# Optimization experiments

Measured on AMD Instinct MI355X. Metric: run time of the kernel, lower is better.

The kernel has to match this reference:

```python
import jax, jax.numpy as jnp
import numpy as np

NUM_OPS = 8
D = 1024
B = 8192


def setup_inputs() -> dict:
    key = jax.random.key(0)
    k1, k2, k3, k4 = jax.random.split(key, 4)
    x = jax.random.normal(k1, (B, D), dtype=jnp.float32)
    logits = 0.001 * jax.random.normal(k2, (NUM_OPS,), dtype=jnp.float32)
    Ws = jax.random.normal(k3, (NUM_OPS, D, D), dtype=jnp.float32) * (1.0 / np.sqrt(D))
    bs = jax.random.normal(k4, (NUM_OPS, D), dtype=jnp.float32) * 0.01
    return {"x": x, "logits": logits, "Ws": Ws, "bs": bs, "num_on_samples": 2}


def reference(x, logits, Ws, bs, num_on_samples):
    # non_stochastic_call: top-k op selection by architecture logits,
    # dispatch x to the selected ops, sum-combine the results.
    _, top_k_ids = jax.lax.top_k(logits, num_on_samples)  # [k]
    W_sel = jnp.take(Ws, top_k_ids, axis=0)  # [k, D, D]
    b_sel = jnp.take(bs, top_k_ids, axis=0)  # [k, D]
    # each op is Dense(D->D) + relu: [k, B, D]
    op_results = jax.nn.relu(jnp.einsum('bd,kde->kbe', x, W_sel) + b_sel[:, None, :])
    return jnp.sum(op_results, axis=0)  # [B, D]
```

## Files before the change

kernel.cpp:

```cpp
#include <hip/hip_runtime.h>
#include <hip/hip_bf16.h>

#define NUM_OPS 8
#define D 1024
#define B_ROWS 8192

typedef unsigned short ushort_t;
typedef __attribute__((ext_vector_type(8))) short bf16x8;
typedef __attribute__((ext_vector_type(4))) float f32x4;
typedef __attribute__((ext_vector_type(4))) float float4v;
typedef __attribute__((ext_vector_type(8))) unsigned short ushort8;

__device__ __forceinline__ unsigned short f2bf(float f) {
    union { float f; unsigned int u; } v; v.f = f;
    unsigned int u = v.u;
    unsigned int lsb = (u >> 16) & 1u;
    u += 0x7fffu + lsb;
    return (unsigned short)(u >> 16);
}

__device__ __forceinline__ void load_lds16(const void* g, void* l) {
    __builtin_amdgcn_global_load_lds(
        (const __attribute__((address_space(1))) void*)g,
        (__attribute__((address_space(3))) void*)l,
        16, 0, 0);
}

__device__ __forceinline__ void top2(const float* __restrict__ logits, int& i0, int& i1) {
    float best = -__builtin_inff(); i0 = 0;
    for (int i = 0; i < NUM_OPS; ++i) { float v = logits[i]; if (v > best) { best = v; i0 = i; } }
    float best2 = -__builtin_inff(); i1 = 0;
    for (int i = 0; i < NUM_OPS; ++i) {
        if (i == i0) continue;
        float v = logits[i]; if (v > best2) { best2 = v; i1 = i; }
    }
}

__global__ void convert_x(const float* __restrict__ x, ushort_t* __restrict__ xb) {
    int i = (blockIdx.x * 256 + threadIdx.x) * 8;
    float4v v0 = *(const float4v*)(x + i);
    float4v v1 = *(const float4v*)(x + i + 4);
    ushort8 o;
    o[0] = f2bf(v0[0]); o[1] = f2bf(v0[1]); o[2] = f2bf(v0[2]); o[3] = f2bf(v0[3]);
    o[4] = f2bf(v1[0]); o[5] = f2bf(v1[1]); o[6] = f2bf(v1[2]); o[7] = f2bf(v1[3]);
    *(ushort8*)(xb + i) = o;
}

__global__ void gather_transpose_W(const float* __restrict__ Ws,
                                   const float* __restrict__ logits,
                                   ushort_t* __restrict__ Wt) {
    __shared__ float t[32][33];
    int i0, i1; top2(logits, i0, i1);
    int e    = blockIdx.x >> 10;
    int tile = blockIdx.x & 1023;
    int td = (tile >> 5) << 5;
    int te = (tile & 31) << 5;
    int tx = threadIdx.x & 31, ty = threadIdx.x >> 5;
    const float* W = Ws + (size_t)(e ? i1 : i0) * D * D;
    for (int r = 0; r < 4; ++r)
        t[ty + 8 * r][tx] = W[(size_t)(td + ty + 8 * r) * D + te + tx];
    __syncthreads();
    ushort_t* o = Wt + (size_t)e * D * D;
    for (int r = 0; r < 4; ++r)
        o[(size_t)(te + ty + 8 * r) * D + td + tx] = f2bf(t[tx][ty + 8 * r]);
}

__device__ __forceinline__ void stageA(const ushort_t* __restrict__ xbf, int brow,
                                       int u, ushort_t* dst, int tid) {
    #pragma unroll
    for (int q = 0; q < 4; ++q) {
        const int c   = q * 512 + tid;
        const int rr  = c >> 3;
        const int gcb = ((c & 7) * 16) ^ ((rr & 7) << 4);
        load_lds16(xbf + (size_t)(brow + rr) * D + u * 64 + (gcb >> 1), dst + c * 8);
    }
}
__device__ __forceinline__ void stageB(const ushort_t* __restrict__ Wt, int bcol,
                                       int u, ushort_t* dst, int tid) {
    #pragma unroll
    for (int q = 0; q < 2; ++q) {
        const int c   = q * 512 + tid;
        const int e   = c >> 9, cc = c & 511;
        const int n   = cc >> 3;
        const int gcb = ((cc & 7) * 16) ^ ((n & 7) << 4);
        load_lds16(Wt + (size_t)e * D * D + (size_t)(bcol + n) * D + u * 64 + (gcb >> 1),
                   dst + c * 8);
    }
}

#define SB()    __builtin_amdgcn_sched_barrier(0)
#define PRIO1() __builtin_amdgcn_s_setprio(1)
#define PRIO0() __builtin_amdgcn_s_setprio(0)

#define TILE(CA, CB, DA, DB, SU, VMN, DOSTG, DOBAR)                                \
    do {                                                                           \
        if (DOSTG) { stageA(xbf, brow, (SU), DA, tid);                             \
                     stageB(Wt,  bcol, (SU), DB, tid); }                           \
        SB();                                                                      \
        bf16x8 a[2][4], b[2][2][2];                                                \
        _Pragma("unroll") for (int kk = 0; kk < 2; ++kk)                           \
        _Pragma("unroll") for (int m = 0; m < 4; ++m)                              \
            a[kk][m] = *(const bf16x8*)((const char*)(CA) +                        \
                (size_t)((rgrp * 64 + m * 16 + l15) * 128) + (kk ? x1 : x0));      \
        _Pragma("unroll") for (int e = 0; e < 2; ++e)                              \
        _Pragma("unroll") for (int kk = 0; kk < 2; ++kk)                           \
        _Pragma("unroll") for (int n16 = 0; n16 < 2; ++n16)                        \
            b[e][kk][n16] = *(const bf16x8*)((const char*)(CB) + e * 8192 +        \
                (size_t)((cgrp * 32 + n16 * 16 + l15) * 128) + (kk ? x1 : x0));    \
        PRIO1();                                                                   \
        _Pragma("unroll") for (int kk = 0; kk < 2; ++kk)                           \
        _Pragma("unroll") for (int e = 0; e < 2; ++e)                              \
        _Pragma("unroll") for (int m = 0; m < 4; ++m)                              \
        _Pragma("unroll") for (int n16 = 0; n16 < 2; ++n16)                        \
            acc[e][m][n16] = __builtin_amdgcn_mfma_f32_16x16x32_bf16(              \
                a[kk][m], b[e][kk][n16], acc[e][m][n16], 0, 0, 0);                 \
        PRIO0();                                                                   \
        SB();                                                                      \
        asm volatile("s_waitcnt vmcnt(" #VMN ")" ::: "memory");                    \
        if (DOBAR) __builtin_amdgcn_s_barrier();                                   \
    } while (0)

__global__ __launch_bounds__(512, 2)
void gemm_dual(const ushort_t* __restrict__ xbf, const ushort_t* __restrict__ Wt,
               const float* __restrict__ bs, const float* __restrict__ logits,
               float* __restrict__ out) {
    __shared__ __align__(16) ushort_t As0[256 * 64], As1[256 * 64], As2[256 * 64];
    __shared__ __align__(16) ushort_t Bs0[2 * 64 * 64], Bs1[2 * 64 * 64], Bs2[2 * 64 * 64];

    const int tid  = threadIdx.x;
    const int wv   = tid >> 6;
    const int lane = tid & 63;
    const int rgrp = wv >> 1, cgrp = wv & 1;
    const int l15  = lane & 15, lq = lane >> 4;
    const int swz  = (l15 & 7) << 4;
    const int x0   = (lq * 16) ^ swz;
    const int x1   = (64 + lq * 16) ^ swz;

    const int bid  = blockIdx.x;
    const int brow = (bid & 31) * 256;
    const int bcol = (bid >> 5) * 64;

    f32x4 acc[2][4][2] = {};

    stageA(xbf, brow, 0, As0, tid); stageB(Wt, bcol, 0, Bs0, tid);
    stageA(xbf, brow, 1, As1, tid); stageB(Wt, bcol, 1, Bs1, tid);
    SB();
    asm volatile("s_waitcnt vmcnt(6)" ::: "memory");
    __builtin_amdgcn_s_barrier();

    TILE(As0, Bs0, As2, Bs2,  2, 6, true,  true);
    TILE(As1, Bs1, As0, Bs0,  3, 6, true,  true);
    TILE(As2, Bs2, As1, Bs1,  4, 6, true,  true);
    TILE(As0, Bs0, As2, Bs2,  5, 6, true,  true);
    TILE(As1, Bs1, As0, Bs0,  6, 6, true,  true);
    TILE(As2, Bs2, As1, Bs1,  7, 6, true,  true);
    TILE(As0, Bs0, As2, Bs2,  8, 6, true,  true);
    TILE(As1, Bs1, As0, Bs0,  9, 6, true,  true);
    TILE(As2, Bs2, As1, Bs1, 10, 6, true,  true);
    TILE(As0, Bs0, As2, Bs2, 11, 6, true,  true);
    TILE(As1, Bs1, As0, Bs0, 12, 6, true,  true);
    TILE(As2, Bs2, As1, Bs1, 13, 6, true,  true);
    TILE(As0, Bs0, As2, Bs2, 14, 6, true,  true);
    TILE(As1, Bs1, As0, Bs0, 15, 6, true,  true);
    TILE(As2, Bs2, As0, Bs0,  0, 0, false, true);
    TILE(As0, Bs0, As1, Bs1,  0, 0, false, false);

    int i0, i1; top2(logits, i0, i1);
    #pragma unroll
    for (int n16 = 0; n16 < 2; ++n16) {
        const int col = bcol + cgrp * 32 + n16 * 16 + l15;
        const float b0 = bs[i0 * D + col];
        const float b1 = bs[i1 * D + col];
        #pragma unroll
        for (int m = 0; m < 4; ++m) {
            const int rbase = brow + rgrp * 64 + m * 16 + lq * 4;
            #pragma unroll
            for (int i = 0; i < 4; ++i) {
                float v0 = acc[0][m][n16][i] + b0; v0 = v0 > 0.f ? v0 : 0.f;
                float v1 = acc[1][m][n16][i] + b1; v1 = v1 > 0.f ? v1 : 0.f;
                out[(size_t)(rbase + i) * D + col] = v0 + v1;
            }
        }
    }
}

extern "C" void kernel_launch(void* const* d_in, const int* in_sizes, int n_in,
                              void* d_out, int out_size, void* d_ws, size_t ws_size,
                              hipStream_t stream) {
    const float* x      = (const float*)d_in[0];
    const float* logits = (const float*)d_in[1];
    const float* Ws     = (const float*)d_in[2];
    const float* bs     = (const float*)d_in[3];
    float* out = (float*)d_out;

    char* ws = (char*)d_ws;
    ushort_t* xbf = (ushort_t*)ws;
    ushort_t* Wt  = (ushort_t*)(ws + (size_t)B_ROWS * D * 2);

    convert_x<<<(B_ROWS * D) / (256 * 8), 256, 0, stream>>>(x, xbf);
    gather_transpose_W<<<2 * (D / 32) * (D / 32), 256, 0, stream>>>(Ws, logits, Wt);

    gemm_dual<<<512, 512, 0, stream>>>(xbf, Wt, bs, logits, out);
}
```

Baseline: 52.66 us.

## Pre-swizzle W into MFMA fragment layout and load B directly to registers

The W gather kernel now writes bf16 weights in per-lane MFMA fragment order, so the GEMM loads B operands straight from global memory into registers and skips LDS staging. The GEMM block changes from 512 threads over a 256x64 tile to 256 threads over a 128x128 tile, with each wave computing 64x64 per expert and double-buffering its B fragments in registers. This removes B's LDS traffic and barriers, and it shrinks shared memory. In exchange it uses more registers, since the accumulators double, and it relies on global/L2 latency for B being hidden.

```diff
diff --git a/kernel.cpp b/kernel.cpp
--- a/kernel.cpp
+++ b/kernel.cpp
@@ -46,138 +46,152 @@
     *(ushort8*)(xb + i) = o;
 }
 
-__global__ void gather_transpose_W(const float* __restrict__ Ws,
-                                   const float* __restrict__ logits,
-                                   ushort_t* __restrict__ Wt) {
+__global__ void gather_frag_W(const float* __restrict__ Ws,
+                              const float* __restrict__ logits,
+                              ushort_t* __restrict__ Wf) {
     __shared__ float t[32][33];
-    int i0, i1; top2(logits, i0, i1);
-    int e    = blockIdx.x >> 10;
-    int tile = blockIdx.x & 1023;
-    int td = (tile >> 5) << 5;
-    int te = (tile & 31) << 5;
-    int tx = threadIdx.x & 31, ty = threadIdx.x >> 5;
-    const float* W = Ws + (size_t)(e ? i1 : i0) * D * D;
+    int s0, s1; top2(logits, s0, s1);
+    const int b  = blockIdx.x;
+    const int nt = b & 31, kt = (b >> 5) & 31, e = b >> 10;
+    const int td = kt * 32, te = nt * 32;
+    const int tx = threadIdx.x & 31, ty = threadIdx.x >> 5;
+    const float* W = Ws + (size_t)(e ? s1 : s0) * D * D;
+    #pragma unroll
     for (int r = 0; r < 4; ++r)
         t[ty + 8 * r][tx] = W[(size_t)(td + ty + 8 * r) * D + te + tx];
     __syncthreads();
-    ushort_t* o = Wt + (size_t)e * D * D;
-    for (int r = 0; r < 4; ++r)
-        o[(size_t)(te + ty + 8 * r) * D + td + tx] = f2bf(t[tx][ty + 8 * r]);
+    const int vid = threadIdx.x;
+    if (vid < 128) {
+        const int n_l = vid & 31, kg = vid >> 5;
+        const int n = te + n_l, k0 = td + kg * 8;
+        const int u = k0 >> 6, kk = (k0 >> 5) & 1, lq = (k0 >> 3) & 3;
+        const int P = n >> 6, c4 = (n >> 4) & 3, l15 = n & 15;
+        const int lane = lq * 16 + l15;
+        const int fi = ((e * 16 + P) * 16 + u) * 8 + c4 * 2 + kk;
+        ushort8 o;
+        #pragma unroll
+        for (int j = 0; j < 8; ++j) o[j] = f2bf(t[kg * 8 + j][n_l]);
+        *(ushort8*)(Wf + (size_t)fi * 512 + lane * 8) = o;
+    }
 }
 
 __device__ __forceinline__ void stageA(const ushort_t* __restrict__ xbf, int brow,
                                        int u, ushort_t* dst, int tid) {
     #pragma unroll
     for (int q = 0; q < 4; ++q) {
-        const int c   = q * 512 + tid;
+        const int c   = q * 256 + tid;
         const int rr  = c >> 3;
         const int gcb = ((c & 7) * 16) ^ ((rr & 7) << 4);
         load_lds16(xbf + (size_t)(brow + rr) * D + u * 64 + (gcb >> 1), dst + c * 8);
     }
 }
-__device__ __forceinline__ void stageB(const ushort_t* __restrict__ Wt, int bcol,
-                                       int u, ushort_t* dst, int tid) {
-    #pragma unroll
-    for (int q = 0; q < 2; ++q) {
-        const int c   = q * 512 + tid;
-        const int e   = c >> 9, cc = c & 511;
-        const int n   = cc >> 3;
-        const int gcb = ((cc & 7) * 16) ^ ((n & 7) << 4);
-        load_lds16(Wt + (size_t)e * D * D + (size_t)(bcol + n) * D + u * 64 + (gcb >> 1),
-                   dst + c * 8);
-    }
-}
 
 #define SB()    __builtin_amdgcn_sched_barrier(0)
 #define PRIO1() __builtin_amdgcn_s_setprio(1)
 #define PRIO0() __builtin_amdgcn_s_setprio(0)
-
-#define TILE(CA, CB, DA, DB, SU, VMN, DOSTG, DOBAR)                                \
-    do {                                                                           \
-        if (DOSTG) { stageA(xbf, brow, (SU), DA, tid);                             \
-                     stageB(Wt,  bcol, (SU), DB, tid); }                           \
-        SB();                                                                      \
-        bf16x8 a[2][4], b[2][2][2];                                                \
+#define VM(N)   do { asm volatile("s_waitcnt vmcnt(" #N ")" ::: "memory"); } while (0)
+
+#define RD_A(CA)                                                                   \
+    do {                                                                           \
         _Pragma("unroll") for (int kk = 0; kk < 2; ++kk)                           \
         _Pragma("unroll") for (int m = 0; m < 4; ++m)                              \
             a[kk][m] = *(const bf16x8*)((const char*)(CA) +                        \
-                (size_t)((rgrp * 64 + m * 16 + l15) * 128) + (kk ? x1 : x0));      \
-        _Pragma("unroll") for (int e = 0; e < 2; ++e)                              \
-        _Pragma("unroll") for (int kk = 0; kk < 2; ++kk)                           \
-        _Pragma("unroll") for (int n16 = 0; n16 < 2; ++n16)                        \
-            b[e][kk][n16] = *(const bf16x8*)((const char*)(CB) + e * 8192 +        \
-                (size_t)((cgrp * 32 + n16 * 16 + l15) * 128) + (kk ? x1 : x0));    \
+                (size_t)((wr * 64 + m * 16 + l15) * 128) + (kk ? x1 : x0));        \
+    } while (0)
+
+#define LD_B(SET, E, U)                                                            \
+    do {                                                                           \
+        const ushort_t* cb = Wf + ((size_t)(((E) * 16 + P) * 16 + (U)) * 8) * 512  \
+                              + lane * 8;                                          \
+        _Pragma("unroll") for (int i = 0; i < 8; ++i)                              \
+            SET[i] = *(const bf16x8*)(cb + (size_t)i * 512);                       \
+    } while (0)
+
+#define MM(E, SET)                                                                 \
+    do {                                                                           \
         PRIO1();                                                                   \
         _Pragma("unroll") for (int kk = 0; kk < 2; ++kk)                           \
-        _Pragma("unroll") for (int e = 0; e < 2; ++e)                              \
         _Pragma("unroll") for (int m = 0; m < 4; ++m)                              \
-        _Pragma("unroll") for (int n16 = 0; n16 < 2; ++n16)                        \
-            acc[e][m][n16] = __builtin_amdgcn_mfma_f32_16x16x32_bf16(              \
-                a[kk][m], b[e][kk][n16], acc[e][m][n16], 0, 0, 0);                 \
+        _Pragma("unroll") for (int c4 = 0; c4 < 4; ++c4)                           \
+            acc[E][m][c4] = __builtin_amdgcn_mfma_f32_16x16x32_bf16(               \
+                a[kk][m], SET[c4 * 2 + kk], acc[E][m][c4], 0, 0, 0);               \
         PRIO0();                                                                   \
+    } while (0)
+
+#define TILE(CA, DA, SU, U, VMN, DOSTG, DOBAR)                                     \
+    do {                                                                           \
+        RD_A(CA);                                                                  \
+        LD_B(bY, 1, (U));                                                          \
+        if (DOSTG) stageA(xbf, brow, (SU), DA, tid);                               \
         SB();                                                                      \
-        asm volatile("s_waitcnt vmcnt(" #VMN ")" ::: "memory");                    \
+        MM(0, bX);                                                                 \
+        if ((U) < 15) LD_B(bX, 0, (U) + 1);                                        \
+        SB();                                                                      \
+        MM(1, bY);                                                                 \
+        VM(VMN);                                                                   \
         if (DOBAR) __builtin_amdgcn_s_barrier();                                   \
     } while (0)
 
-__global__ __launch_bounds__(512, 2)
-void gemm_dual(const ushort_t* __restrict__ xbf, const ushort_t* __restrict__ Wt,
+__global__ __launch_bounds__(256, 2)
+void gemm_dual(const ushort_t* __restrict__ xbf, const ushort_t* __restrict__ Wf,
                const float* __restrict__ bs, const float* __restrict__ logits,
                float* __restrict__ out) {
-    __shared__ __align__(16) ushort_t As0[256 * 64], As1[256 * 64], As2[256 * 64];
-    __shared__ __align__(16) ushort_t Bs0[2 * 64 * 64], Bs1[2 * 64 * 64], Bs2[2 * 64 * 64];
+    __shared__ __align__(16) ushort_t As0[128 * 64], As1[128 * 64], As2[128 * 64];
 
     const int tid  = threadIdx.x;
     const int wv   = tid >> 6;
     const int lane = tid & 63;
-    const int rgrp = wv >> 1, cgrp = wv & 1;
+    const int wr   = wv >> 1, wc = wv & 1;
     const int l15  = lane & 15, lq = lane >> 4;
     const int swz  = (l15 & 7) << 4;
     const int x0   = (lq * 16) ^ swz;
     const int x1   = (64 + lq * 16) ^ swz;
 
     const int bid  = blockIdx.x;
-    const int brow = (bid & 31) * 256;
-    const int bcol = (bid >> 5) * 64;
-
-    f32x4 acc[2][4][2] = {};
-
-    stageA(xbf, brow, 0, As0, tid); stageB(Wt, bcol, 0, Bs0, tid);
-    stageA(xbf, brow, 1, As1, tid); stageB(Wt, bcol, 1, Bs1, tid);
+    const int brow = (bid & 63) * 128;
+    const int P    = (bid >> 6) * 2 + wc;
+
+    f32x4  acc[2][4][4] = {};
+    bf16x8 a[2][4];
+    bf16x8 bX[8], bY[8];
+
+    stageA(xbf, brow, 0, As0, tid);
+    stageA(xbf, brow, 1, As1, tid);
+    LD_B(bX, 0, 0);
     SB();
-    asm volatile("s_waitcnt vmcnt(6)" ::: "memory");
+    VM(12);
     __builtin_amdgcn_s_barrier();
 
-    TILE(As0, Bs0, As2, Bs2,  2, 6, true,  true);
-    TILE(As1, Bs1, As0, Bs0,  3, 6, true,  true);
-    TILE(As2, Bs2, As1, Bs1,  4, 6, true,  true);
-    TILE(As0, Bs0, As2, Bs2,  5, 6, true,  true);
-    TILE(As1, Bs1, As0, Bs0,  6, 6, true,  true);
-    TILE(As2, Bs2, As1, Bs1,  7, 6, true,  true);
-    TILE(As0, Bs0, As2, Bs2,  8, 6, true,  true);
-    TILE(As1, Bs1, As0, Bs0,  9, 6, true,  true);
-    TILE(As2, Bs2, As1, Bs1, 10, 6, true,  true);
-    TILE(As0, Bs0, As2, Bs2, 11, 6, true,  true);
-    TILE(As1, Bs1, As0, Bs0, 12, 6, true,  true);
-    TILE(As2, Bs2, As1, Bs1, 13, 6, true,  true);
-    TILE(As0, Bs0, As2, Bs2, 14, 6, true,  true);
-    TILE(As1, Bs1, As0, Bs0, 15, 6, true,  true);
-    TILE(As2, Bs2, As0, Bs0,  0, 0, false, true);
-    TILE(As0, Bs0, As1, Bs1,  0, 0, false, false);
-
-    int i0, i1; top2(logits, i0, i1);
+    TILE(As0, As2,  2,  0, 12, true,  true);
+    TILE(As1, As0,  3,  1, 12, true,  true);
+    TILE(As2, As1,  4,  2, 12, true,  true);
+    TILE(As0, As2,  5,  3, 12, true,  true);
+    TILE(As1, As0,  6,  4, 12, true,  true);
+    TILE(As2, As1,  7,  5, 12, true,  true);
+    TILE(As0, As2,  8,  6, 12, true,  true);
+    TILE(As1, As0,  9,  7, 12, true,  true);
+    TILE(As2, As1, 10,  8, 12, true,  true);
+    TILE(As0, As2, 11,  9, 12, true,  true);
+    TILE(As1, As0, 12, 10, 12, true,  true);
+    TILE(As2, As1, 13, 11, 12, true,  true);
+    TILE(As0, As2, 14, 12, 12, true,  true);
+    TILE(As1, As0, 15, 13, 12, true,  true);
+    TILE(As2, As1,  0, 14,  8, false, true);
+    TILE(As0, As1,  0, 15,  0, false, false);
+
+    int s0, s1; top2(logits, s0, s1);
     #pragma unroll
-    for (int n16 = 0; n16 < 2; ++n16) {
-        const int col = bcol + cgrp * 32 + n16 * 16 + l15;
-        const float b0 = bs[i0 * D + col];
-        const float b1 = bs[i1 * D + col];
+    for (int c4 = 0; c4 < 4; ++c4) {
+        const int col = P * 64 + c4 * 16 + l15;
+        const float b0 = bs[s0 * D + col];
+        const float b1 = bs[s1 * D + col];
         #pragma unroll
         for (int m = 0; m < 4; ++m) {
-            const int rbase = brow + rgrp * 64 + m * 16 + lq * 4;
+            const int rbase = brow + wr * 64 + m * 16 + lq * 4;
             #pragma unroll
             for (int i = 0; i < 4; ++i) {
-                float v0 = acc[0][m][n16][i] + b0; v0 = v0 > 0.f ? v0 : 0.f;
-                float v1 = acc[1][m][n16][i] + b1; v1 = v1 > 0.f ? v1 : 0.f;
+                float v0 = acc[0][m][c4][i] + b0; v0 = v0 > 0.f ? v0 : 0.f;
+                float v1 = acc[1][m][c4][i] + b1; v1 = v1 > 0.f ? v1 : 0.f;
                 out[(size_t)(rbase + i) * D + col] = v0 + v1;
             }
         }
@@ -195,10 +209,10 @@
 
     char* ws = (char*)d_ws;
     ushort_t* xbf = (ushort_t*)ws;
-    ushort_t* Wt  = (ushort_t*)(ws + (size_t)B_ROWS * D * 2);
+    ushort_t* Wf  = (ushort_t*)(ws + (size_t)B_ROWS * D * 2);
 
     convert_x<<<(B_ROWS * D) / (256 * 8), 256, 0, stream>>>(x, xbf);
-    gather_transpose_W<<<2 * (D / 32) * (D / 32), 256, 0, stream>>>(Ws, logits, Wt);
-
-    gemm_dual<<<512, 512, 0, stream>>>(xbf, Wt, bs, logits, out);
-}
+    gather_frag_W<<<2 * 32 * 32, 256, 0, stream>>>(Ws, logits, Wf);
+
+    gemm_dual<<<512, 256, 0, stream>>>(xbf, Wf, bs, logits, out);
+}
```

Result: no change. 53.34 us (+1.3%).

## Widen GEMM column tile to 128 and restructure B/A staging pipeline

Applied to the files above, without the earlier changes.

The block tile's N dimension grows from 64 to 128 columns, so each block covers twice the output and the grid halves to 256 blocks. Each wave now computes a 64x64 patch per expert, doubling the accumulators, and A tiles are reused across more columns. B now uses two LDS buffers instead of three and is staged one step ahead, offset from A. Expert-1 B fragments are loaded mid-tile to interleave LDS reads with MFMAs. This raises register pressure and leaves fewer blocks than CUs to fill, which risks occupancy and load imbalance.

```diff
diff --git a/kernel.cpp b/kernel.cpp
--- a/kernel.cpp
+++ b/kernel.cpp
@@ -78,11 +78,11 @@
 __device__ __forceinline__ void stageB(const ushort_t* __restrict__ Wt, int bcol,
                                        int u, ushort_t* dst, int tid) {
     #pragma unroll
-    for (int q = 0; q < 2; ++q) {
+    for (int q = 0; q < 4; ++q) {
         const int c   = q * 512 + tid;
-        const int e   = c >> 9, cc = c & 511;
-        const int n   = cc >> 3;
-        const int gcb = ((cc & 7) * 16) ^ ((n & 7) << 4);
+        const int rr  = c >> 3;
+        const int e   = rr >> 7, n = rr & 127;
+        const int gcb = ((c & 7) * 16) ^ ((rr & 7) << 4);
         load_lds16(Wt + (size_t)e * D * D + (size_t)(bcol + n) * D + u * 64 + (gcb >> 1),
                    dst + c * 8);
     }
@@ -91,33 +91,39 @@
 #define SB()    __builtin_amdgcn_sched_barrier(0)
 #define PRIO1() __builtin_amdgcn_s_setprio(1)
 #define PRIO0() __builtin_amdgcn_s_setprio(0)
-
-#define TILE(CA, CB, DA, DB, SU, VMN, DOSTG, DOBAR)                                \
+#define VMN(N)  do { asm volatile("s_waitcnt vmcnt(" #N ")" ::: "memory"); SB(); } while (0)
+
+#define MM16(E, KK, BB)                                                            \
     do {                                                                           \
-        if (DOSTG) { stageA(xbf, brow, (SU), DA, tid);                             \
-                     stageB(Wt,  bcol, (SU), DB, tid); }                           \
-        SB();                                                                      \
-        bf16x8 a[2][4], b[2][2][2];                                                \
+        _Pragma("unroll") for (int m = 0; m < 4; ++m)                              \
+        _Pragma("unroll") for (int n = 0; n < 4; ++n)                              \
+            acc[E][m][n] = __builtin_amdgcn_mfma_f32_16x16x32_bf16(                \
+                a[KK][m], BB[KK][n], acc[E][m][n], 0, 0, 0);                       \
+    } while (0)
+
+#define TILE(CA, CB, DB, DA, SUB, SUA, STGB, STGA, VN, DOBAR)                      \
+    do {                                                                           \
+        bf16x8 a[2][4], b0[2][4], b1[2][4];                                        \
         _Pragma("unroll") for (int kk = 0; kk < 2; ++kk)                           \
         _Pragma("unroll") for (int m = 0; m < 4; ++m)                              \
             a[kk][m] = *(const bf16x8*)((const char*)(CA) +                        \
-                (size_t)((rgrp * 64 + m * 16 + l15) * 128) + (kk ? x1 : x0));      \
-        _Pragma("unroll") for (int e = 0; e < 2; ++e)                              \
+                (size_t)((wr * 64 + m * 16 + l15) * 128) + (kk ? x1 : x0));        \
         _Pragma("unroll") for (int kk = 0; kk < 2; ++kk)                           \
-        _Pragma("unroll") for (int n16 = 0; n16 < 2; ++n16)                        \
-            b[e][kk][n16] = *(const bf16x8*)((const char*)(CB) + e * 8192 +        \
-                (size_t)((cgrp * 32 + n16 * 16 + l15) * 128) + (kk ? x1 : x0));    \
-        PRIO1();                                                                   \
+        _Pragma("unroll") for (int n = 0; n < 4; ++n)                              \
+            b0[kk][n] = *(const bf16x8*)((const char*)(CB) +                       \
+                (size_t)((wc * 64 + n * 16 + l15) * 128) + (kk ? x1 : x0));        \
+        if (STGB) stageB(Wt,  bcol, (SUB), DB, tid);                               \
+        if (STGA) stageA(xbf, brow, (SUA), DA, tid);                               \
+        SB();                                                                      \
+        PRIO1(); MM16(0, 0, b0); PRIO0();                                          \
         _Pragma("unroll") for (int kk = 0; kk < 2; ++kk)                           \
-        _Pragma("unroll") for (int e = 0; e < 2; ++e)                              \
-        _Pragma("unroll") for (int m = 0; m < 4; ++m)                              \
-        _Pragma("unroll") for (int n16 = 0; n16 < 2; ++n16)                        \
-            acc[e][m][n16] = __builtin_amdgcn_mfma_f32_16x16x32_bf16(              \
-                a[kk][m], b[e][kk][n16], acc[e][m][n16], 0, 0, 0);                 \
-        PRIO0();                                                                   \
+        _Pragma("unroll") for (int n = 0; n < 4; ++n)                              \
+            b1[kk][n] = *(const bf16x8*)((const char*)(CB) + 16384 +               \
+                (size_t)((wc * 64 + n * 16 + l15) * 128) + (kk ? x1 : x0));        \
+        PRIO1(); MM16(0, 1, b0); MM16(1, 0, b1); MM16(1, 1, b1); PRIO0();          \
         SB();                                                                      \
-        asm volatile("s_waitcnt vmcnt(" #VMN ")" ::: "memory");                    \
-        if (DOBAR) __builtin_amdgcn_s_barrier();                                   \
+        VMN(VN);                                                                   \
+        if (DOBAR) { __builtin_amdgcn_s_barrier(); SB(); }                         \
     } while (0)
 
 __global__ __launch_bounds__(512, 2)
@@ -125,12 +131,12 @@
                const float* __restrict__ bs, const float* __restrict__ logits,
                float* __restrict__ out) {
     __shared__ __align__(16) ushort_t As0[256 * 64], As1[256 * 64], As2[256 * 64];
-    __shared__ __align__(16) ushort_t Bs0[2 * 64 * 64], Bs1[2 * 64 * 64], Bs2[2 * 64 * 64];
+    __shared__ __align__(16) ushort_t Bs0[256 * 64], Bs1[256 * 64];
 
     const int tid  = threadIdx.x;
     const int wv   = tid >> 6;
     const int lane = tid & 63;
-    const int rgrp = wv >> 1, cgrp = wv & 1;
+    const int wr   = wv >> 1, wc = wv & 1;
     const int l15  = lane & 15, lq = lane >> 4;
     const int swz  = (l15 & 7) << 4;
     const int x0   = (lq * 16) ^ swz;
@@ -138,46 +144,47 @@
 
     const int bid  = blockIdx.x;
     const int brow = (bid & 31) * 256;
-    const int bcol = (bid >> 5) * 64;
-
-    f32x4 acc[2][4][2] = {};
-
-    stageA(xbf, brow, 0, As0, tid); stageB(Wt, bcol, 0, Bs0, tid);
-    stageA(xbf, brow, 1, As1, tid); stageB(Wt, bcol, 1, Bs1, tid);
+    const int bcol = (bid >> 5) * 128;
+
+    f32x4 acc[2][4][4] = {};
+
+    stageB(Wt,  bcol, 0, Bs0, tid);
+    stageA(xbf, brow, 0, As0, tid);
+    stageA(xbf, brow, 1, As1, tid);
     SB();
-    asm volatile("s_waitcnt vmcnt(6)" ::: "memory");
-    __builtin_amdgcn_s_barrier();
-
-    TILE(As0, Bs0, As2, Bs2,  2, 6, true,  true);
-    TILE(As1, Bs1, As0, Bs0,  3, 6, true,  true);
-    TILE(As2, Bs2, As1, Bs1,  4, 6, true,  true);
-    TILE(As0, Bs0, As2, Bs2,  5, 6, true,  true);
-    TILE(As1, Bs1, As0, Bs0,  6, 6, true,  true);
-    TILE(As2, Bs2, As1, Bs1,  7, 6, true,  true);
-    TILE(As0, Bs0, As2, Bs2,  8, 6, true,  true);
-    TILE(As1, Bs1, As0, Bs0,  9, 6, true,  true);
-    TILE(As2, Bs2, As1, Bs1, 10, 6, true,  true);
-    TILE(As0, Bs0, As2, Bs2, 11, 6, true,  true);
-    TILE(As1, Bs1, As0, Bs0, 12, 6, true,  true);
-    TILE(As2, Bs2, As1, Bs1, 13, 6, true,  true);
-    TILE(As0, Bs0, As2, Bs2, 14, 6, true,  true);
-    TILE(As1, Bs1, As0, Bs0, 15, 6, true,  true);
-    TILE(As2, Bs2, As0, Bs0,  0, 0, false, true);
-    TILE(As0, Bs0, As1, Bs1,  0, 0, false, false);
+    VMN(4);
+    __builtin_amdgcn_s_barrier(); SB();
+
+    TILE(As0, Bs0, Bs1, As2,  1,  2, true,  true,  4, true);
+    TILE(As1, Bs1, Bs0, As0,  2,  3, true,  true,  4, true);
+    TILE(As2, Bs0, Bs1, As1,  3,  4, true,  true,  4, true);
+    TILE(As0, Bs1, Bs0, As2,  4,  5, true,  true,  4, true);
+    TILE(As1, Bs0, Bs1, As0,  5,  6, true,  true,  4, true);
+    TILE(As2, Bs1, Bs0, As1,  6,  7, true,  true,  4, true);
+    TILE(As0, Bs0, Bs1, As2,  7,  8, true,  true,  4, true);
+    TILE(As1, Bs1, Bs0, As0,  8,  9, true,  true,  4, true);
+    TILE(As2, Bs0, Bs1, As1,  9, 10, true,  true,  4, true);
+    TILE(As0, Bs1, Bs0, As2, 10, 11, true,  true,  4, true);
+    TILE(As1, Bs0, Bs1, As0, 11, 12, true,  true,  4, true);
+    TILE(As2, Bs1, Bs0, As1, 12, 13, true,  true,  4, true);
+    TILE(As0, Bs0, Bs1, As2, 13, 14, true,  true,  4, true);
+    TILE(As1, Bs1, Bs0, As0, 14, 15, true,  true,  4, true);
+    TILE(As2, Bs0, Bs1, As1, 15,  0, true,  false, 0, true);
+    TILE(As0, Bs1, Bs0, As1,  0,  0, false, false, 0, false);
 
     int i0, i1; top2(logits, i0, i1);
     #pragma unroll
-    for (int n16 = 0; n16 < 2; ++n16) {
-        const int col = bcol + cgrp * 32 + n16 * 16 + l15;
+    for (int n = 0; n < 4; ++n) {
+        const int col = bcol + wc * 64 + n * 16 + l15;
         const float b0 = bs[i0 * D + col];
         const float b1 = bs[i1 * D + col];
         #pragma unroll
         for (int m = 0; m < 4; ++m) {
-            const int rbase = brow + rgrp * 64 + m * 16 + lq * 4;
+            const int rbase = brow + wr * 64 + m * 16 + lq * 4;
             #pragma unroll
             for (int i = 0; i < 4; ++i) {
-                float v0 = acc[0][m][n16][i] + b0; v0 = v0 > 0.f ? v0 : 0.f;
-                float v1 = acc[1][m][n16][i] + b1; v1 = v1 > 0.f ? v1 : 0.f;
+                float v0 = acc[0][m][n][i] + b0; v0 = v0 > 0.f ? v0 : 0.f;
+                float v1 = acc[1][m][n][i] + b1; v1 = v1 > 0.f ? v1 : 0.f;
                 out[(size_t)(rbase + i) * D + col] = v0 + v1;
             }
         }
@@ -200,5 +207,5 @@
     convert_x<<<(B_ROWS * D) / (256 * 8), 256, 0, stream>>>(x, xbf);
     gather_transpose_W<<<2 * (D / 32) * (D / 32), 256, 0, stream>>>(Ws, logits, Wt);
 
-    gemm_dual<<<512, 512, 0, stream>>>(xbf, Wt, bs, logits, out);
-}
+    gemm_dual<<<256, 512, 0, stream>>>(xbf, Wt, bs, logits, out);
+}
```

After: 57.76 us. 1.1x slower.

## Double-buffer LDS-to-register fragments to overlap reads with MFMA

Applied to the files above, without the earlier changes.

Restructures the main GEMM loop so each tile reads the next tile's A/B fragments from LDS into a second register set while MFMAs run on the previously loaded fragments. Synchronisation moves to the start of each tile as a full vmcnt(0) wait plus barrier, replacing the partial vmcnt(6) wait at the end. This hides LDS read latency behind matrix math. In exchange it doubles fragment register usage under launch bounds of 512 threads with 2 blocks per CU, and the stricter vmcnt(0) wait may expose global-load latency.

```diff
diff --git a/kernel.cpp b/kernel.cpp
--- a/kernel.cpp
+++ b/kernel.cpp
@@ -91,33 +91,42 @@
 #define SB()    __builtin_amdgcn_sched_barrier(0)
 #define PRIO1() __builtin_amdgcn_s_setprio(1)
 #define PRIO0() __builtin_amdgcn_s_setprio(0)
-
-#define TILE(CA, CB, DA, DB, SU, VMN, DOSTG, DOBAR)                                \
+#define VM0()   do { asm volatile("s_waitcnt vmcnt(0)" ::: "memory"); } while (0)
+
+#define READF(AF, BF, CA, CB)                                                      \
     do {                                                                           \
-        if (DOSTG) { stageA(xbf, brow, (SU), DA, tid);                             \
-                     stageB(Wt,  bcol, (SU), DB, tid); }                           \
-        SB();                                                                      \
-        bf16x8 a[2][4], b[2][2][2];                                                \
         _Pragma("unroll") for (int kk = 0; kk < 2; ++kk)                           \
         _Pragma("unroll") for (int m = 0; m < 4; ++m)                              \
-            a[kk][m] = *(const bf16x8*)((const char*)(CA) +                        \
+            AF[kk][m] = *(const bf16x8*)((const char*)(CA) +                       \
                 (size_t)((rgrp * 64 + m * 16 + l15) * 128) + (kk ? x1 : x0));      \
         _Pragma("unroll") for (int e = 0; e < 2; ++e)                              \
         _Pragma("unroll") for (int kk = 0; kk < 2; ++kk)                           \
         _Pragma("unroll") for (int n16 = 0; n16 < 2; ++n16)                        \
-            b[e][kk][n16] = *(const bf16x8*)((const char*)(CB) + e * 8192 +        \
+            BF[e][kk][n16] = *(const bf16x8*)((const char*)(CB) + e * 8192 +       \
                 (size_t)((cgrp * 32 + n16 * 16 + l15) * 128) + (kk ? x1 : x0));    \
+    } while (0)
+
+#define MM32(AF, BF)                                                               \
+    do {                                                                           \
         PRIO1();                                                                   \
         _Pragma("unroll") for (int kk = 0; kk < 2; ++kk)                           \
         _Pragma("unroll") for (int e = 0; e < 2; ++e)                              \
         _Pragma("unroll") for (int m = 0; m < 4; ++m)                              \
         _Pragma("unroll") for (int n16 = 0; n16 < 2; ++n16)                        \
             acc[e][m][n16] = __builtin_amdgcn_mfma_f32_16x16x32_bf16(              \
-                a[kk][m], b[e][kk][n16], acc[e][m][n16], 0, 0, 0);                 \
+                AF[kk][m], BF[e][kk][n16], acc[e][m][n16], 0, 0, 0);               \
         PRIO0();                                                                   \
+    } while (0)
+
+#define TILE(FR_A, FR_B, SLOT_RA, SLOT_RB, FC_A, FC_B, SU, DA, DB, DORD, DOSTG)    \
+    do {                                                                           \
+        VM0();                                                                     \
+        __builtin_amdgcn_s_barrier();                                              \
+        if (DORD) READF(FR_A, FR_B, SLOT_RA, SLOT_RB);                             \
+        if (DOSTG) { stageA(xbf, brow, (SU), DA, tid);                             \
+                     stageB(Wt,  bcol, (SU), DB, tid); }                           \
         SB();                                                                      \
-        asm volatile("s_waitcnt vmcnt(" #VMN ")" ::: "memory");                    \
-        if (DOBAR) __builtin_amdgcn_s_barrier();                                   \
+        MM32(FC_A, FC_B);                                                          \
     } while (0)
 
 __global__ __launch_bounds__(512, 2)
@@ -141,43 +150,47 @@
     const int bcol = (bid >> 5) * 64;
 
     f32x4 acc[2][4][2] = {};
+    bf16x8 a0[2][4], b0[2][2][2];
+    bf16x8 a1[2][4], b1[2][2][2];
 
     stageA(xbf, brow, 0, As0, tid); stageB(Wt, bcol, 0, Bs0, tid);
     stageA(xbf, brow, 1, As1, tid); stageB(Wt, bcol, 1, Bs1, tid);
     SB();
     asm volatile("s_waitcnt vmcnt(6)" ::: "memory");
     __builtin_amdgcn_s_barrier();
-
-    TILE(As0, Bs0, As2, Bs2,  2, 6, true,  true);
-    TILE(As1, Bs1, As0, Bs0,  3, 6, true,  true);
-    TILE(As2, Bs2, As1, Bs1,  4, 6, true,  true);
-    TILE(As0, Bs0, As2, Bs2,  5, 6, true,  true);
-    TILE(As1, Bs1, As0, Bs0,  6, 6, true,  true);
-    TILE(As2, Bs2, As1, Bs1,  7, 6, true,  true);
-    TILE(As0, Bs0, As2, Bs2,  8, 6, true,  true);
-    TILE(As1, Bs1, As0, Bs0,  9, 6, true,  true);
-    TILE(As2, Bs2, As1, Bs1, 10, 6, true,  true);
-    TILE(As0, Bs0, As2, Bs2, 11, 6, true,  true);
-    TILE(As1, Bs1, As0, Bs0, 12, 6, true,  true);
-    TILE(As2, Bs2, As1, Bs1, 13, 6, true,  true);
-    TILE(As0, Bs0, As2, Bs2, 14, 6, true,  true);
-    TILE(As1, Bs1, As0, Bs0, 15, 6, true,  true);
-    TILE(As2, Bs2, As0, Bs0,  0, 0, false, true);
-    TILE(As0, Bs0, As1, Bs1,  0, 0, false, false);
+    READF(a0, b0, As0, Bs0);
+    SB();
+
+    TILE(a1, b1, As1, Bs1, a0, b0,  2, As2, Bs2, true,  true);
+    TILE(a0, b0, As2, Bs2, a1, b1,  3, As0, Bs0, true,  true);
+    TILE(a1, b1, As0, Bs0, a0, b0,  4, As1, Bs1, true,  true);
+    TILE(a0, b0, As1, Bs1, a1, b1,  5, As2, Bs2, true,  true);
+    TILE(a1, b1, As2, Bs2, a0, b0,  6, As0, Bs0, true,  true);
+    TILE(a0, b0, As0, Bs0, a1, b1,  7, As1, Bs1, true,  true);
+    TILE(a1, b1, As1, Bs1, a0, b0,  8, As2, Bs2, true,  true);
+    TILE(a0, b0, As2, Bs2, a1, b1,  9, As0, Bs0, true,  true);
+    TILE(a1, b1, As0, Bs0, a0, b0, 10, As1, Bs1, true,  true);
+    TILE(a0, b0, As1, Bs1, a1, b1, 11, As2, Bs2, true,  true);
+    TILE(a1, b1, As2, Bs2, a0, b0, 12, As0, Bs0, true,  true);
+    TILE(a0, b0, As0, Bs0, a1, b1, 13, As1, Bs1, true,  true);
+    TILE(a1, b1, As1, Bs1, a0, b0, 14, As2, Bs2, true,  true);
+    TILE(a0, b0, As2, Bs2, a1, b1, 15, As0, Bs0, true,  true);
+    TILE(a1, b1, As0, Bs0, a0, b0,  0, As0, Bs0, true,  false);
+    TILE(a0, b0, As0, Bs0, a1, b1,  0, As0, Bs0, false, false);
 
     int i0, i1; top2(logits, i0, i1);
     #pragma unroll
     for (int n16 = 0; n16 < 2; ++n16) {
         const int col = bcol + cgrp * 32 + n16 * 16 + l15;
-        const float b0 = bs[i0 * D + col];
-        const float b1 = bs[i1 * D + col];
+        const float bb0 = bs[i0 * D + col];
+        const float bb1 = bs[i1 * D + col];
         #pragma unroll
         for (int m = 0; m < 4; ++m) {
             const int rbase = brow + rgrp * 64 + m * 16 + lq * 4;
             #pragma unroll
             for (int i = 0; i < 4; ++i) {
-                float v0 = acc[0][m][n16][i] + b0; v0 = v0 > 0.f ? v0 : 0.f;
-                float v1 = acc[1][m][n16][i] + b1; v1 = v1 > 0.f ? v1 : 0.f;
+                float v0 = acc[0][m][n16][i] + bb0; v0 = v0 > 0.f ? v0 : 0.f;
+                float v1 = acc[1][m][n16][i] + bb1; v1 = v1 > 0.f ? v1 : 0.f;
                 out[(size_t)(rbase + i) * D + col] = v0 + v1;
             }
         }
```

New measurement: 53.99 us. 1.03x slower.
